# Performance work log

Hardware: AMD Instinct MI355X
Metric: run time of the kernel (lower is better)

## Reference

```python
import jax, jax.numpy as jnp
import numpy as np

N = 100000
E = 1600000
IN_F = 128
H_F = 128


def _sage_layer(h, weights, src, dst, W_self, b_self, W_neigh):
    # message: w_e * h[src]  -> [E, F]
    m = h[src] * weights[:, None]
    # segment-mean over destination nodes (DGL fn.mean divides by in-degree)
    s = jax.ops.segment_sum(m, dst, num_segments=N)
    deg = jax.ops.segment_sum(jnp.ones((E,), h.dtype), dst, num_segments=N)
    neigh = s / jnp.maximum(deg, 1.0)[:, None]
    # DGL SAGEConv('mean'): fc_self(h) + fc_neigh(neigh); bias lives in fc_self
    return h @ W_self.T + b_self + neigh @ W_neigh.T


def setup_inputs() -> dict:
    key = jax.random.key(0)
    ks = jax.random.split(key, 10)
    scale_in = 1.0 / np.sqrt(IN_F)
    scale_h = 1.0 / np.sqrt(H_F)
    return {
        "in_feat": jax.random.normal(ks[0], (N, IN_F), jnp.float32),
        "weights": jax.random.uniform(ks[1], (E,), jnp.float32),
        "src": jax.random.randint(ks[2], (E,), 0, N),
        "dst": jax.random.randint(ks[3], (E,), 0, N),
        "W_self1": jax.random.normal(ks[4], (H_F, IN_F), jnp.float32) * scale_in,
        "b_self1": jnp.zeros((H_F,), jnp.float32),
        "W_neigh1": jax.random.normal(ks[5], (H_F, IN_F), jnp.float32) * scale_in,
        "W_self2": jax.random.normal(ks[6], (H_F, H_F), jnp.float32) * scale_h,
        "b_self2": jnp.zeros((H_F,), jnp.float32),
        "W_neigh2": jax.random.normal(ks[7], (H_F, H_F), jnp.float32) * scale_h,
    }


def reference(in_feat, weights, src, dst, W_self1, b_self1, W_neigh1, W_self2, b_self2, W_neigh2):
    h = _sage_layer(in_feat, weights, src, dst, W_self1, b_self1, W_neigh1)
    h = jax.nn.relu(h)
    h = _sage_layer(h, weights, src, dst, W_self2, b_self2, W_neigh2)
    return h
```

## Files before the change

### kernel.cpp

```cpp
#include <hip/hip_runtime.h>


#define NN 100000
#define NE 1600000
#define F 128

#define NPB 128
#define NPB_BITS 7
#define NBUK ((NN + NPB - 1) / NPB)
#define EPB 4096
#define NBLK3 ((NE + EPB - 1) / EPB)
#define EPB2 8192
#define NBLK2 ((NE + EPB2 - 1) / EPB2)

#define CONV_BLOCKS 6250

static const size_t BBASE_OFF = 0;
static const size_t BCUR_OFF  = 4000;
static const size_t BCNT_OFF  = 8000;
static const size_t ROW_OFF   = 12000;
static const size_t EDGE_OFF  = 804112;
static const size_t WCAT1_OFF = 13604112;
static const size_t WCAT2_OFF = 13669648;
static const size_t SBF_OFF   = 13735184;
static const size_t H1BF_OFF  = 39335184;
static const size_t WS_NEED   = 64935184;

static const size_t FB_S_OFF = 524288;

typedef __attribute__((ext_vector_type(8))) short short8;
typedef __attribute__((ext_vector_type(4))) float float4v;

__device__ __forceinline__ float bf2f(unsigned int u16) {
    unsigned int x = u16 << 16;
    float f;
    __builtin_memcpy(&f, &x, 4);
    return f;
}
__device__ __forceinline__ unsigned int f2bf(float f) {
    unsigned int x;
    __builtin_memcpy(&x, &f, 4);
    unsigned int r = x + 0x7FFFu + ((x >> 16) & 1u);
    return r >> 16;
}

__device__ __forceinline__ void gload_lds16(const unsigned short* g, unsigned short* l) {
    __builtin_amdgcn_global_load_lds(
        (const __attribute__((address_space(1))) unsigned int*)(g),
        (__attribute__((address_space(3))) unsigned int*)(l), 16, 0, 0);
}


__global__ __launch_bounds__(256) void bcount_kernel(const int* __restrict__ dst,
                                                     int* __restrict__ bcnt) {
    __shared__ int hist[NBUK];
    int t = threadIdx.x;
    for (int i = t; i < NBUK; i += 256) hist[i] = 0;
    __syncthreads();
    int base_e = blockIdx.x * EPB2;
#pragma unroll
    for (int i = 0; i < EPB2 / 256; i++) {
        int e = base_e + i * 256 + t;
        if (e < NE) atomicAdd(&hist[dst[e] >> NPB_BITS], 1);
    }
    __syncthreads();
    for (int i = t; i < NBUK; i += 256) {
        int h = hist[i];
        if (h) atomicAdd(&bcnt[i], h);
    }
}

__global__ __launch_bounds__(256) void bscan_kernel(const int* __restrict__ bcnt,
                                                    int* __restrict__ bbase,
                                                    int* __restrict__ bcur) {
    __shared__ int ts[256];
    int t = threadIdx.x;
    int v[4];
    int base = t * 4;
    int s = 0;
#pragma unroll
    for (int i = 0; i < 4; i++) {
        int idx = base + i;
        v[i] = (idx < NBUK) ? bcnt[idx] : 0;
        s += v[i];
    }
    ts[t] = s;
    __syncthreads();
    for (int off = 1; off < 256; off <<= 1) {
        int u = (t >= off) ? ts[t - off] : 0;
        __syncthreads();
        ts[t] += u;
        __syncthreads();
    }
    int run = ts[t] - s;
#pragma unroll
    for (int i = 0; i < 4; i++) {
        int idx = base + i;
        if (idx < NBUK) { bbase[idx] = run; bcur[idx] = run; }
        run += v[i];
    }
    if (t == 255) bbase[NBUK] = run;
}

__global__ __launch_bounds__(256) void bscatter(const int* __restrict__ src,
                                                const int* __restrict__ dst,
                                                const float* __restrict__ w,
                                                int* __restrict__ bcur,
                                                int2* __restrict__ ebuf) {
    __shared__ int2 rec[EPB];
    __shared__ unsigned short bid[EPB];
    __shared__ int hist[NBUK];
    __shared__ int gbase[NBUK];
    __shared__ int cur[NBUK];

    int t = threadIdx.x;
    for (int i = t; i < NBUK; i += 256) { hist[i] = 0; cur[i] = 0; }
    __syncthreads();

    int base_e = blockIdx.x * EPB;
#pragma unroll
    for (int i = 0; i < EPB / 256; i++) {
        int idx = i * 256 + t;
        int e = base_e + idx;
        if (e < NE) {
            int d = dst[e];
            int b = d >> NPB_BITS;
            int2 r;
            r.x = src[e] | ((d & (NPB - 1)) << 17);
            r.y = __float_as_int(w[e]);
            rec[idx] = r;
            bid[idx] = (unsigned short)b;
            atomicAdd(&hist[b], 1);
        } else {
            bid[idx] = 0xFFFFu;
        }
    }
    __syncthreads();

    for (int i = t; i < NBUK; i += 256)
        if (hist[i] > 0) gbase[i] = atomicAdd(&bcur[i], hist[i]);
    __syncthreads();

#pragma unroll
    for (int i = 0; i < EPB / 256; i++) {
        int idx = i * 256 + t;
        int b = bid[idx];
        if (b != 0xFFFFu) {
            int r = atomicAdd(&cur[b], 1);
            ebuf[gbase[b] + r] = rec[idx];
        }
    }
}

__global__ __launch_bounds__(256) void fine_fill2(const int* __restrict__ bbase,
                                                  const int2* __restrict__ ebuf,
                                                  int* __restrict__ row,
                                                  int2* __restrict__ edge) {
    __shared__ int lcnt[NPB];
    __shared__ int ts[NPB];
    __shared__ int lcur[NPB];
    int b = blockIdx.x;
    int t = threadIdx.x;
    int n0 = b * NPB;

    if (t < NPB) lcnt[t] = 0;
    __syncthreads();

    int beg = bbase[b], end = bbase[b + 1];

    for (int e = beg + t; e < end; e += 256) {
        int dl = (ebuf[e].x >> 17) & (NPB - 1);
        atomicAdd(&lcnt[dl], 1);
    }
    __syncthreads();

    int v = (t < NPB) ? lcnt[t] : 0;
    if (t < NPB) ts[t] = v;
    __syncthreads();
    for (int off = 1; off < NPB; off <<= 1) {
        int u = (t >= off && t < NPB) ? ts[t - off] : 0;
        __syncthreads();
        if (t < NPB) ts[t] += u;
        __syncthreads();
    }
    if (t < NPB) {
        int o = beg + ts[t] - v;
        lcur[t] = o;
        int n = n0 + t;
        if (n <= NN) row[n] = o;
    }
    __syncthreads();

    for (int e = beg + t; e < end; e += 256) {
        int2 r = ebuf[e];
        int dl = (r.x >> 17) & (NPB - 1);
        int pos = atomicAdd(&lcur[dl], 1);
        int2 o;
        o.x = r.x & 0x1FFFF;
        o.y = r.y;
        edge[pos] = o;
    }
}

__global__ __launch_bounds__(256) void prep_kernel(const float* __restrict__ in,
                                                   unsigned short* __restrict__ outbf,
                                                   const float* __restrict__ Ws1,
                                                   const float* __restrict__ Wn1,
                                                   const float* __restrict__ Ws2,
                                                   const float* __restrict__ Wn2,
                                                   unsigned short* __restrict__ wcat1,
                                                   unsigned short* __restrict__ wcat2) {
    if (blockIdx.x < CONV_BLOCKS) {
        size_t base = ((size_t)blockIdx.x * 256 + threadIdx.x) * 8;
        float4 a = *(const float4*)(in + base);
        float4 b = *(const float4*)(in + base + 4);
        uint4 p;
        p.x = f2bf(a.x) | (f2bf(a.y) << 16);
        p.y = f2bf(a.z) | (f2bf(a.w) << 16);
        p.z = f2bf(b.x) | (f2bf(b.y) << 16);
        p.w = f2bf(b.z) | (f2bf(b.w) << 16);
        *(uint4*)(outbf + base) = p;
    } else {
        int idx = (blockIdx.x - CONV_BLOCKS) * 256 + threadIdx.x;
        int which = idx >> 15;
        int j = idx & 32767;
        int n = j >> 8, k = j & 255;
        const float* Ws = which ? Ws2 : Ws1;
        const float* Wn = which ? Wn2 : Wn1;
        float v = (k < 128) ? Ws[n * 128 + k] : Wn[n * 128 + (k - 128)];
        unsigned short* o = which ? wcat2 : wcat1;
        o[j] = (unsigned short)f2bf(v);
    }
}

__global__ __launch_bounds__(256) void gather_packed(const unsigned short* __restrict__ h,
                                                     const int* __restrict__ row,
                                                     const int2* __restrict__ edge,
                                                     unsigned short* __restrict__ sbf) {
    int t = threadIdx.x;
    int lane = t & 63;
    int n = blockIdx.x * 4 + (t >> 6);
    int beg = __builtin_amdgcn_readfirstlane(row[n]);
    int end = __builtin_amdgcn_readfirstlane(row[n + 1]);
    const unsigned int* hp = (const unsigned int*)h;

    float ax = 0.0f, ay = 0.0f;
    int e = beg;
    for (; e + 7 < end; e += 8) {
        int2 m[8];
#pragma unroll
        for (int i = 0; i < 8; i++) m[i] = edge[e + i];
        unsigned int p[8];
#pragma unroll
        for (int i = 0; i < 8; i++) p[i] = hp[(size_t)m[i].x * 64 + lane];
#pragma unroll
        for (int i = 0; i < 8; i++) {
            float wf = __int_as_float(m[i].y);
            ax += wf * bf2f(p[i] & 0xFFFFu);
            ay += wf * bf2f(p[i] >> 16);
        }
    }
    for (; e < end; e++) {
        int2 m0 = edge[e];
        unsigned int p0 = hp[(size_t)m0.x * 64 + lane];
        float wf = __int_as_float(m0.y);
        ax += wf * bf2f(p0 & 0xFFFFu);
        ay += wf * bf2f(p0 >> 16);
    }
    float invd = 1.0f / fmaxf((float)(end - beg), 1.0f);
    unsigned int outp = f2bf(ax * invd) | (f2bf(ay * invd) << 16);
    ((unsigned int*)sbf)[(size_t)n * 64 + lane] = outp;
}


__global__ __launch_bounds__(512, 4) void mfma_gemm(
    const unsigned short* self_bf,
    const unsigned short* __restrict__ sbf,
    const unsigned short* __restrict__ wcat,
    const float* __restrict__ bias,
    unsigned short* out_bf,
    float* __restrict__ out_f32)
{
    __shared__ unsigned short Bs[128][256];

    int t = threadIdx.x;
    int l = t & 63;
    int w = t >> 6;
    int base = blockIdx.x * 256;
    int lane16 = l & 15;
    int quad = l >> 4;
    int swz = (lane16 & 7) << 3;

    unsigned short* lbase = &Bs[0][0];
#pragma unroll
    for (int i = 0; i < 8; i++) {
        int idx = i * 512 + t;
        int r = idx >> 5;
        int cb = (idx & 31) << 4;
        int sb = cb ^ ((r & 7) << 4);
        gload_lds16(wcat + r * 256 + (sb >> 1), lbase + idx * 8);
    }

    int r0 = base + w * 32 + lane16;
    int r1 = r0 + 16;
    int r0c = min(r0, NN - 1);
    int r1c = min(r1, NN - 1);

    float4v acc0[8], acc1[8];
#pragma unroll
    for (int ct = 0; ct < 8; ct++) {
        acc0[ct] = (float4v){0.f, 0.f, 0.f, 0.f};
        acc1[ct] = (float4v){0.f, 0.f, 0.f, 0.f};
    }

    __syncthreads();

#pragma unroll
    for (int half = 0; half < 2; half++) {
        const unsigned short* srcb = (half == 0) ? self_bf : sbf;
        const unsigned short* p0 = srcb + (size_t)r0c * F + quad * 8;
        const unsigned short* p1 = srcb + (size_t)r1c * F + quad * 8;
        short8 Ah0[4], Ah1[4];
#pragma unroll
        for (int kk = 0; kk < 4; kk++) {
            Ah0[kk] = *(const short8*)(p0 + kk * 32);
            Ah1[kk] = *(const short8*)(p1 + kk * 32);
        }
#pragma unroll
        for (int kk = 0; kk < 4; kk++) {
#pragma unroll
            for (int ct = 0; ct < 8; ct++) {
                int r = ct * 16 + lane16;
                int col = half * 128 + kk * 32 + quad * 8;
                short8 b = *(const short8*)(lbase + (size_t)r * 256 + (col ^ swz));
                acc0[ct] = __builtin_amdgcn_mfma_f32_16x16x32_bf16(Ah0[kk], b, acc0[ct], 0, 0, 0);
                acc1[ct] = __builtin_amdgcn_mfma_f32_16x16x32_bf16(Ah1[kk], b, acc1[ct], 0, 0, 0);
            }
        }
    }

    int rowb0 = base + w * 32 + quad * 4;
    int rowb1 = rowb0 + 16;
#pragma unroll
    for (int ct = 0; ct < 8; ct++) {
        int col = ct * 16 + lane16;
        float bc = bias[col];
#pragma unroll
        for (int r = 0; r < 4; r++) {
            int g0 = rowb0 + r, g1 = rowb1 + r;
            float v0 = acc0[ct][r] + bc;
            float v1 = acc1[ct][r] + bc;
            if (out_bf) {
                v0 = fmaxf(v0, 0.0f);
                v1 = fmaxf(v1, 0.0f);
                if (g0 < NN) out_bf[(size_t)g0 * F + col] = (unsigned short)f2bf(v0);
                if (g1 < NN) out_bf[(size_t)g1 * F + col] = (unsigned short)f2bf(v1);
            } else {
                if (g0 < NN) out_f32[(size_t)g0 * F + col] = v0;
                if (g1 < NN) out_f32[(size_t)g1 * F + col] = v1;
            }
        }
    }
}


__global__ __launch_bounds__(256) void scatter_kernel(const float* __restrict__ h,
                                                      const float* __restrict__ w,
                                                      const int* __restrict__ src,
                                                      const int* __restrict__ dst,
                                                      float* __restrict__ s,
                                                      float* __restrict__ deg,
                                                      int add_deg) {
    int e = blockIdx.x * 4 + (threadIdx.x >> 6);
    int lane = threadIdx.x & 63;
    int sn = src[e];
    int dn = dst[e];
    float wf = w[e];
    float2 p = *(const float2*)(h + (size_t)sn * F + lane * 2);
    float* sp = s + (size_t)dn * F + lane * 2;
    unsafeAtomicAdd(sp,     wf * p.x);
    unsafeAtomicAdd(sp + 1, wf * p.y);
    if (add_deg && lane == 0) unsafeAtomicAdd(&deg[dn], 1.0f);
}

__global__ __launch_bounds__(256) void sage_gemm(const float* h,
                                                 const float* __restrict__ s,
                                                 const float* deg,
                                                 const float* __restrict__ Ws,
                                                 const float* __restrict__ bias,
                                                 const float* __restrict__ Wn,
                                                 float* out,
                                                 int relu) {
    __shared__ float xs[16][F];
    __shared__ float invd[16];
    int t = threadIdx.x;
    int j = t & 127;
    int g = t >> 7;
    int base = blockIdx.x * 16;
    for (int idx = t; idx < 16 * 32; idx += 256) {
        int n = idx >> 5, kq = idx & 31;
        *(float4*)&xs[n][kq * 4] = *(const float4*)(h + (size_t)(base + n) * F + kq * 4);
    }
    if (t < 16) invd[t] = deg ? 1.0f / fmaxf(deg[base + t], 1.0f) : 1.0f;
    __syncthreads();
    float acc[8];
#pragma unroll
    for (int i = 0; i < 8; i++) acc[i] = 0.0f;
    for (int kc = 0; kc < F; kc += 4) {
        float4 wv = *(const float4*)(Ws + j * F + kc);
#pragma unroll
        for (int i = 0; i < 8; i++) {
            const float* xr = &xs[g * 8 + i][kc];
            acc[i] += xr[0] * wv.x + xr[1] * wv.y + xr[2] * wv.z + xr[3] * wv.w;
        }
    }
    __syncthreads();
    for (int idx = t; idx < 16 * 32; idx += 256) {
        int n = idx >> 5, kq = idx & 31;
        float4 sv = *(const float4*)(s + (size_t)(base + n) * F + kq * 4);
        float iv = invd[n];
        xs[n][kq * 4]     = sv.x * iv;
        xs[n][kq * 4 + 1] = sv.y * iv;
        xs[n][kq * 4 + 2] = sv.z * iv;
        xs[n][kq * 4 + 3] = sv.w * iv;
    }
    __syncthreads();
    for (int kc = 0; kc < F; kc += 4) {
        float4 wv = *(const float4*)(Wn + j * F + kc);
#pragma unroll
        for (int i = 0; i < 8; i++) {
            const float* xr = &xs[g * 8 + i][kc];
            acc[i] += xr[0] * wv.x + xr[1] * wv.y + xr[2] * wv.z + xr[3] * wv.w;
        }
    }
    float bj = bias[j];
#pragma unroll
    for (int i = 0; i < 8; i++) {
        int n = base + g * 8 + i;
        float v = acc[i] + bj;
        if (relu) v = fmaxf(v, 0.0f);
        out[(size_t)n * F + j] = v;
    }
}

extern "C" void kernel_launch(void* const* d_in, const int* in_sizes, int n_in,
                              void* d_out, int out_size, void* d_ws, size_t ws_size,
                              hipStream_t stream) {
    const float* in_feat = (const float*)d_in[0];
    const float* weights = (const float*)d_in[1];
    const int* src = (const int*)d_in[2];
    const int* dst = (const int*)d_in[3];
    const float* Ws1 = (const float*)d_in[4];
    const float* b1  = (const float*)d_in[5];
    const float* Wn1 = (const float*)d_in[6];
    const float* Ws2 = (const float*)d_in[7];
    const float* b2  = (const float*)d_in[8];
    const float* Wn2 = (const float*)d_in[9];
    float* out = (float*)d_out;

    if (ws_size >= WS_NEED) {
        int* bbase  = (int*)((char*)d_ws + BBASE_OFF);
        int* bcur   = (int*)((char*)d_ws + BCUR_OFF);
        int* bcnt   = (int*)((char*)d_ws + BCNT_OFF);
        int* row    = (int*)((char*)d_ws + ROW_OFF);
        int2* edge  = (int2*)((char*)d_ws + EDGE_OFF);
        unsigned short* wcat1 = (unsigned short*)((char*)d_ws + WCAT1_OFF);
        unsigned short* wcat2 = (unsigned short*)((char*)d_ws + WCAT2_OFF);
        unsigned short* sbf   = (unsigned short*)((char*)d_ws + SBF_OFF);
        int2* ebuf  = (int2*)((char*)d_ws + SBF_OFF);
        unsigned short* hbf   = (unsigned short*)((char*)d_ws + H1BF_OFF);

        hipMemsetAsync(bcnt, 0, NBUK * sizeof(int), stream);
        bcount_kernel<<<NBLK2, 256, 0, stream>>>(dst, bcnt);
        bscan_kernel<<<1, 256, 0, stream>>>(bcnt, bbase, bcur);
        bscatter<<<NBLK3, 256, 0, stream>>>(src, dst, weights, bcur, ebuf);
        fine_fill2<<<NBUK, 256, 0, stream>>>(bbase, ebuf, row, edge);
        prep_kernel<<<CONV_BLOCKS + 256, 256, 0, stream>>>(in_feat, hbf,
                                                           Ws1, Wn1, Ws2, Wn2,
                                                           wcat1, wcat2);

        gather_packed<<<NN / 4, 256, 0, stream>>>(hbf, row, edge, sbf);
        mfma_gemm<<<(NN + 255) / 256, 512, 0, stream>>>(hbf, sbf, wcat1, b1, hbf, nullptr);
        gather_packed<<<NN / 4, 256, 0, stream>>>(hbf, row, edge, sbf);
        mfma_gemm<<<(NN + 255) / 256, 512, 0, stream>>>(hbf, sbf, wcat2, b2, nullptr, out);
    } else {
        float* deg = (float*)d_ws;
        float* s   = (float*)((char*)d_ws + FB_S_OFF);
        hipMemsetAsync(d_ws, 0, FB_S_OFF + (size_t)NN * F * 4, stream);
        scatter_kernel<<<NE / 4, 256, 0, stream>>>(in_feat, weights, src, dst, s, deg, 1);
        sage_gemm<<<NN / 16, 256, 0, stream>>>(in_feat, s, deg, Ws1, b1, Wn1, out, 1);
        hipMemsetAsync(s, 0, (size_t)NN * F * 4, stream);
        scatter_kernel<<<NE / 4, 256, 0, stream>>>(out, weights, src, dst, s, deg, 0);
        sage_gemm<<<NN / 16, 256, 0, stream>>>(out, s, deg, Ws2, b2, Wn2, out, 0);
    }
}
```

Baseline: 380.3 us.

## Fuse neighbor gather with MFMA GEMM per layer into one kernel

Replaces the separate gather_packed and mfma_gemm kernels with a fused kernel. Each wave aggregates 16 destination rows into a swizzled LDS tile, then runs the self and neighbor MFMA products directly from that tile. This removes the sbf intermediate write and read round trip and two launches per forward pass. In exchange, weights are read straight from global memory instead of being staged in LDS, and a separate h1 buffer replaces the in-place update. Each wave also processes its 16 rows serially during the gather phase, which may reduce memory-level parallelism.

Measured after the change: 480.0 us. 26.2% more time.

```diff
diff --git a/kernel.cpp b/kernel.cpp
--- a/kernel.cpp
+++ b/kernel.cpp
@@ -14,6 +14,7 @@
 #define NBLK2 ((NE + EPB2 - 1) / EPB2)
 
 #define CONV_BLOCKS 6250
+#define GG_BLOCKS ((NN + 63) / 64)
 
 static const size_t BBASE_OFF = 0;
 static const size_t BCUR_OFF  = 4000;
@@ -22,7 +23,7 @@
 static const size_t EDGE_OFF  = 804112;
 static const size_t WCAT1_OFF = 13604112;
 static const size_t WCAT2_OFF = 13669648;
-static const size_t SBF_OFF   = 13735184;
+static const size_t H1_OFF    = 13735184;
 static const size_t H1BF_OFF  = 39335184;
 static const size_t WS_NEED   = 64935184;
 
@@ -42,12 +43,6 @@
     __builtin_memcpy(&x, &f, 4);
     unsigned int r = x + 0x7FFFu + ((x >> 16) & 1u);
     return r >> 16;
-}
-
-__device__ __forceinline__ void gload_lds16(const unsigned short* g, unsigned short* l) {
-    __builtin_amdgcn_global_load_lds(
-        (const __attribute__((address_space(1))) unsigned int*)(g),
-        (__attribute__((address_space(3))) unsigned int*)(l), 16, 0, 0);
 }
 
 
@@ -233,131 +228,108 @@
     }
 }
 
-__global__ __launch_bounds__(256) void gather_packed(const unsigned short* __restrict__ h,
-                                                     const int* __restrict__ row,
-                                                     const int2* __restrict__ edge,
-                                                     unsigned short* __restrict__ sbf) {
-    int t = threadIdx.x;
-    int lane = t & 63;
-    int n = blockIdx.x * 4 + (t >> 6);
-    int beg = __builtin_amdgcn_readfirstlane(row[n]);
-    int end = __builtin_amdgcn_readfirstlane(row[n + 1]);
-    const unsigned int* hp = (const unsigned int*)h;
-
-    float ax = 0.0f, ay = 0.0f;
-    int e = beg;
-    for (; e + 7 < end; e += 8) {
-        int2 m[8];
-#pragma unroll
-        for (int i = 0; i < 8; i++) m[i] = edge[e + i];
-        unsigned int p[8];
-#pragma unroll
-        for (int i = 0; i < 8; i++) p[i] = hp[(size_t)m[i].x * 64 + lane];
-#pragma unroll
-        for (int i = 0; i < 8; i++) {
-            float wf = __int_as_float(m[i].y);
-            ax += wf * bf2f(p[i] & 0xFFFFu);
-            ay += wf * bf2f(p[i] >> 16);
-        }
-    }
-    for (; e < end; e++) {
-        int2 m0 = edge[e];
-        unsigned int p0 = hp[(size_t)m0.x * 64 + lane];
-        float wf = __int_as_float(m0.y);
-        ax += wf * bf2f(p0 & 0xFFFFu);
-        ay += wf * bf2f(p0 >> 16);
-    }
-    float invd = 1.0f / fmaxf((float)(end - beg), 1.0f);
-    unsigned int outp = f2bf(ax * invd) | (f2bf(ay * invd) << 16);
-    ((unsigned int*)sbf)[(size_t)n * 64 + lane] = outp;
-}
-
-
-__global__ __launch_bounds__(512, 4) void mfma_gemm(
-    const unsigned short* self_bf,
-    const unsigned short* __restrict__ sbf,
+
+__global__ __launch_bounds__(256, 4) void fused_gg(
+    const unsigned short* __restrict__ h,
+    const int* __restrict__ row,
+    const int2* __restrict__ edge,
     const unsigned short* __restrict__ wcat,
     const float* __restrict__ bias,
-    unsigned short* out_bf,
+    unsigned short* __restrict__ out_bf,
     float* __restrict__ out_f32)
 {
-    __shared__ unsigned short Bs[128][256];
-
-    int t = threadIdx.x;
-    int l = t & 63;
+    __shared__ unsigned int tile[4][16][64];
+
+    int t = threadIdx.x;
+    int lane = t & 63;
     int w = t >> 6;
-    int base = blockIdx.x * 256;
-    int lane16 = l & 15;
-    int quad = l >> 4;
-    int swz = (lane16 & 7) << 3;
-
-    unsigned short* lbase = &Bs[0][0];
-#pragma unroll
-    for (int i = 0; i < 8; i++) {
-        int idx = i * 512 + t;
-        int r = idx >> 5;
-        int cb = (idx & 31) << 4;
-        int sb = cb ^ ((r & 7) << 4);
-        gload_lds16(wcat + r * 256 + (sb >> 1), lbase + idx * 8);
-    }
-
-    int r0 = base + w * 32 + lane16;
-    int r1 = r0 + 16;
+    int lane16 = lane & 15;
+    int quad = lane >> 4;
+    int n0w = blockIdx.x * 64 + w * 16;
+
+    const unsigned int* hp = (const unsigned int*)h;
+
+    for (int i = 0; i < 16; i++) {
+        int n = n0w + i;
+        if (n >= NN) break;
+        int beg = __builtin_amdgcn_readfirstlane(row[n]);
+        int end = __builtin_amdgcn_readfirstlane(row[n + 1]);
+
+        float ax = 0.0f, ay = 0.0f;
+        int e = beg;
+        for (; e + 7 < end; e += 8) {
+            int2 m[8];
+#pragma unroll
+            for (int j = 0; j < 8; j++) m[j] = edge[e + j];
+            unsigned int p[8];
+#pragma unroll
+            for (int j = 0; j < 8; j++) p[j] = hp[(size_t)m[j].x * 64 + lane];
+#pragma unroll
+            for (int j = 0; j < 8; j++) {
+                float wf = __int_as_float(m[j].y);
+                ax += wf * bf2f(p[j] & 0xFFFFu);
+                ay += wf * bf2f(p[j] >> 16);
+            }
+        }
+        for (; e < end; e++) {
+            int2 m0 = edge[e];
+            unsigned int p0 = hp[(size_t)m0.x * 64 + lane];
+            float wf = __int_as_float(m0.y);
+            ax += wf * bf2f(p0 & 0xFFFFu);
+            ay += wf * bf2f(p0 >> 16);
+        }
+        float invd = 1.0f / fmaxf((float)(end - beg), 1.0f);
+        unsigned int outp = f2bf(ax * invd) | (f2bf(ay * invd) << 16);
+        tile[w][i][lane ^ ((i & 7) << 2)] = outp;
+    }
+
+    int r0 = n0w + lane16;
     int r0c = min(r0, NN - 1);
-    int r1c = min(r1, NN - 1);
-
-    float4v acc0[8], acc1[8];
-#pragma unroll
-    for (int ct = 0; ct < 8; ct++) {
-        acc0[ct] = (float4v){0.f, 0.f, 0.f, 0.f};
-        acc1[ct] = (float4v){0.f, 0.f, 0.f, 0.f};
-    }
-
-    __syncthreads();
-
-#pragma unroll
-    for (int half = 0; half < 2; half++) {
-        const unsigned short* srcb = (half == 0) ? self_bf : sbf;
-        const unsigned short* p0 = srcb + (size_t)r0c * F + quad * 8;
-        const unsigned short* p1 = srcb + (size_t)r1c * F + quad * 8;
-        short8 Ah0[4], Ah1[4];
-#pragma unroll
-        for (int kk = 0; kk < 4; kk++) {
-            Ah0[kk] = *(const short8*)(p0 + kk * 32);
-            Ah1[kk] = *(const short8*)(p1 + kk * 32);
-        }
-#pragma unroll
-        for (int kk = 0; kk < 4; kk++) {
-#pragma unroll
-            for (int ct = 0; ct < 8; ct++) {
-                int r = ct * 16 + lane16;
-                int col = half * 128 + kk * 32 + quad * 8;
-                short8 b = *(const short8*)(lbase + (size_t)r * 256 + (col ^ swz));
-                acc0[ct] = __builtin_amdgcn_mfma_f32_16x16x32_bf16(Ah0[kk], b, acc0[ct], 0, 0, 0);
-                acc1[ct] = __builtin_amdgcn_mfma_f32_16x16x32_bf16(Ah1[kk], b, acc1[ct], 0, 0, 0);
-            }
-        }
-    }
-
-    int rowb0 = base + w * 32 + quad * 4;
-    int rowb1 = rowb0 + 16;
+    const unsigned short* sp = h + (size_t)r0c * F + quad * 8;
+
+    float4v acc[8];
+#pragma unroll
+    for (int ct = 0; ct < 8; ct++) acc[ct] = (float4v){0.f, 0.f, 0.f, 0.f};
+
+    short8 As[4];
+#pragma unroll
+    for (int kk = 0; kk < 4; kk++) As[kk] = *(const short8*)(sp + kk * 32);
+#pragma unroll
+    for (int kk = 0; kk < 4; kk++) {
+#pragma unroll
+        for (int ct = 0; ct < 8; ct++) {
+            short8 b = *(const short8*)(wcat +
+                (size_t)(ct * 16 + lane16) * 256 + kk * 32 + quad * 8);
+            acc[ct] = __builtin_amdgcn_mfma_f32_16x16x32_bf16(As[kk], b, acc[ct], 0, 0, 0);
+        }
+    }
+
+#pragma unroll
+    for (int kk = 0; kk < 4; kk++) {
+        int ucol = (kk * 16 + quad * 4) ^ ((lane16 & 7) << 2);
+        short8 an = *(const short8*)&tile[w][lane16][ucol];
+#pragma unroll
+        for (int ct = 0; ct < 8; ct++) {
+            short8 b = *(const short8*)(wcat +
+                (size_t)(ct * 16 + lane16) * 256 + 128 + kk * 32 + quad * 8);
+            acc[ct] = __builtin_amdgcn_mfma_f32_16x16x32_bf16(an, b, acc[ct], 0, 0, 0);
+        }
+    }
+
+    int rowb = n0w + quad * 4;
 #pragma unroll
     for (int ct = 0; ct < 8; ct++) {
         int col = ct * 16 + lane16;
         float bc = bias[col];
 #pragma unroll
         for (int r = 0; r < 4; r++) {
-            int g0 = rowb0 + r, g1 = rowb1 + r;
-            float v0 = acc0[ct][r] + bc;
-            float v1 = acc1[ct][r] + bc;
+            int g = rowb + r;
+            float v = acc[ct][r] + bc;
             if (out_bf) {
-                v0 = fmaxf(v0, 0.0f);
-                v1 = fmaxf(v1, 0.0f);
-                if (g0 < NN) out_bf[(size_t)g0 * F + col] = (unsigned short)f2bf(v0);
-                if (g1 < NN) out_bf[(size_t)g1 * F + col] = (unsigned short)f2bf(v1);
+                v = fmaxf(v, 0.0f);
+                if (g < NN) out_bf[(size_t)g * F + col] = (unsigned short)f2bf(v);
             } else {
-                if (g0 < NN) out_f32[(size_t)g0 * F + col] = v0;
-                if (g1 < NN) out_f32[(size_t)g1 * F + col] = v1;
+                if (g < NN) out_f32[(size_t)g * F + col] = v;
             }
         }
     }
@@ -466,8 +438,8 @@
         int2* edge  = (int2*)((char*)d_ws + EDGE_OFF);
         unsigned short* wcat1 = (unsigned short*)((char*)d_ws + WCAT1_OFF);
         unsigned short* wcat2 = (unsigned short*)((char*)d_ws + WCAT2_OFF);
-        unsigned short* sbf   = (unsigned short*)((char*)d_ws + SBF_OFF);
-        int2* ebuf  = (int2*)((char*)d_ws + SBF_OFF);
+        unsigned short* h1    = (unsigned short*)((char*)d_ws + H1_OFF);
+        int2* ebuf  = (int2*)((char*)d_ws + H1_OFF);
         unsigned short* hbf   = (unsigned short*)((char*)d_ws + H1BF_OFF);
 
         hipMemsetAsync(bcnt, 0, NBUK * sizeof(int), stream);
@@ -479,10 +451,8 @@
                                                            Ws1, Wn1, Ws2, Wn2,
                                                            wcat1, wcat2);
 
-        gather_packed<<<NN / 4, 256, 0, stream>>>(hbf, row, edge, sbf);
-        mfma_gemm<<<(NN + 255) / 256, 512, 0, stream>>>(hbf, sbf, wcat1, b1, hbf, nullptr);
-        gather_packed<<<NN / 4, 256, 0, stream>>>(hbf, row, edge, sbf);
-        mfma_gemm<<<(NN + 255) / 256, 512, 0, stream>>>(hbf, sbf, wcat2, b2, nullptr, out);
+        fused_gg<<<GG_BLOCKS, 256, 0, stream>>>(hbf, row, edge, wcat1, b1, h1, nullptr);
+        fused_gg<<<GG_BLOCKS, 256, 0, stream>>>(h1, row, edge, wcat2, b2, nullptr, out);
     } else {
         float* deg = (float*)d_ws;
         float* s   = (float*)((char*)d_ws + FB_S_OFF);
```
